# Kernel tuning notes

Hardware: AMD Instinct MI355X
Metric: run time of the kernel (lower is better)

Reference implementation:

```python
import jax, jax.numpy as jnp
import numpy as np

B, T, N, V, C, E = 64, 100, 25, 128, 128, 64
EPS = 1e-5


def setup_inputs() -> dict:
    key = jax.random.key(0)
    ks = jax.random.split(key, 6)
    x = jax.random.normal(ks[0], (B, T, N, V), jnp.float32)
    edge_index = jax.random.randint(ks[1], (2, E), 0, N, dtype=jnp.int64)
    W1 = jax.random.normal(ks[2], (V, C), jnp.float32) * (1.0 / np.sqrt(V))
    b1 = jnp.zeros((C,), jnp.float32)
    W2 = jax.random.normal(ks[3], (C, C), jnp.float32) * (1.0 / np.sqrt(C))
    b2 = jnp.zeros((C,), jnp.float32)
    gamma = jnp.ones((T,), jnp.float32)
    beta = jnp.zeros((T,), jnp.float32)
    return {"x": x, "edge_index": edge_index, "W1": W1, "b1": b1,
            "W2": W2, "b2": b2, "gamma": gamma, "beta": beta}


def _gcn_norm(edge_index, n):
    # GCNConv default: add self-loops, symmetric D^{-1/2} A_hat D^{-1/2} norm.
    loop = jnp.arange(n, dtype=edge_index.dtype)
    src = jnp.concatenate([edge_index[0], loop])  # [E + N]
    tgt = jnp.concatenate([edge_index[1], loop])
    deg = jnp.zeros((n,), jnp.float32).at[tgt].add(1.0)
    dis = jax.lax.rsqrt(deg)  # deg >= 1 due to self-loops
    return src, tgt, dis[src] * dis[tgt]


def _gcn_layer(h, W, b, src, tgt, norm):
    # h: [G, N, Cin] -> [G, N, Cout]; linear then gather-scale-scatter aggregate.
    h = jnp.einsum('gnc,cd->gnd', h, W)
    msg = h[:, src, :] * norm[None, :, None]          # [G, E+N, Cout]
    out = jnp.zeros_like(h).at[:, tgt, :].add(msg)    # scatter-add to targets
    return out + b


def reference(x, edge_index, W1, b1, W2, b2, gamma, beta):
    Bv, Tv, Nv, Vv = x.shape
    h = x.reshape(Bv * Tv, Nv, Vv)  # B*T independent graphs, shared edge_index
    src, tgt, norm = _gcn_norm(edge_index, Nv)
    h = _gcn_layer(h, W1, b1, src, tgt, norm)
    h = _gcn_layer(h, W2, b2, src, tgt, norm)
    y = h.reshape(Bv, Tv, Nv, -1)
    # BatchNorm2d(T) in training mode: batch stats over (B, N, C) per T-channel.
    mean = y.mean(axis=(0, 2, 3), keepdims=True)
    var = y.var(axis=(0, 2, 3), keepdims=True)  # biased, matches torch normalization
    y = (y - mean) * jax.lax.rsqrt(var + EPS)
    y = y * gamma[None, :, None, None] + beta[None, :, None, None]
    return jax.nn.relu(y)
```

## Files before the change

kernel.cpp:

```cpp
#include <hip/hip_runtime.h>

#define T_DIM   100
#define N_NODES 25
#define C_DIM   128
#define G_TOTAL 6400
#define GNV     3200
#define TOT_ELEM 20480000
#define CNT_PER_T 204800.0f

#define WS_A2P  0
#define WS_RS1  640
#define WS_BW   768
#define WS_SUM  1024
#define WS_SSQ  1152
#define WS_W12T 2048
#define WS_HB   16384

#define YSTR  36
#define YGSTR (128 * YSTR)

typedef __attribute__((ext_vector_type(8))) short short8;
typedef __attribute__((ext_vector_type(4))) float f32x4;

__device__ __forceinline__ unsigned short f2bf(float f) {
  unsigned int u = __float_as_uint(f);
  u += 0x7FFFu + ((u >> 16) & 1u);
  return (unsigned short)(u >> 16);
}
__device__ __forceinline__ float bf2f(unsigned short h) {
  return __uint_as_float(((unsigned int)h) << 16);
}
__device__ __forceinline__ unsigned int pack2bf(float a, float b) {
  return (unsigned int)f2bf(a) | ((unsigned int)f2bf(b) << 16);
}

__global__ void k_pre(const int* __restrict__ edge, const float* __restrict__ W1,
                      const float* __restrict__ W2, const float* __restrict__ b1,
                      float* __restrict__ wsf) {
  __shared__ float sA[N_NODES * N_NODES];
  __shared__ float sA2[N_NODES * N_NODES];
  __shared__ float sdeg[N_NODES];
  __shared__ float sdis[N_NODES];
  const int tid = threadIdx.x;

  if (blockIdx.x < 64) {
    int j = blockIdx.x * 256 + tid;
    int c = j & 127, v = j >> 7;
    float acc = 0.f;
#pragma unroll 8
    for (int u = 0; u < 128; u++) acc = fmaf(W1[v * 128 + u], W2[u * 128 + c], acc);
    ((unsigned short*)(wsf + WS_W12T))[c * 128 + v] = f2bf(acc);
    if (j < 128) {
      float a2 = 0.f;
      for (int u = 0; u < 128; u++) a2 = fmaf(W2[u * 128 + j], b1[u], a2);
      wsf[WS_BW + j] = a2;
    }
    return;
  }

  if (tid < N_NODES) sdeg[tid] = 0.f;
  for (int j = tid; j < N_NODES * N_NODES; j += 256) sA[j] = 0.f;
  __syncthreads();
  if (tid < 64) atomicAdd(&sdeg[edge[64 + tid]], 1.f);
  __syncthreads();
  if (tid < N_NODES) sdis[tid] = rsqrtf(sdeg[tid] + 1.f);
  __syncthreads();
  if (tid < 64) {
    int s = edge[tid], tg = edge[64 + tid];
    atomicAdd(&sA[tg * N_NODES + s], sdis[s] * sdis[tg]);
  }
  __syncthreads();
  if (tid < N_NODES) atomicAdd(&sA[tid * N_NODES + tid], sdis[tid] * sdis[tid]);
  __syncthreads();
  for (int j = tid; j < N_NODES * N_NODES; j += 256) {
    int n = j / N_NODES, m = j - n * N_NODES;
    float acc = 0.f;
    for (int k = 0; k < N_NODES; k++) acc = fmaf(sA[n * N_NODES + k], sA[k * N_NODES + m], acc);
    sA2[j] = acc;
  }
  __syncthreads();
  for (int j = tid; j < 1024; j += 256) {
    int m = j >> 5, k = j & 31;
    float v = (m < N_NODES && k < N_NODES) ? sA2[m * N_NODES + k] : 0.f;
    ((unsigned short*)(wsf + WS_A2P))[j] = f2bf(v);
  }
  if (tid < N_NODES) {
    float rs = 0.f;
    for (int m = 0; m < N_NODES; m++) rs += sA[tid * N_NODES + m];
    wsf[WS_RS1 + tid] = rs;
  }
  if (tid < T_DIM) { wsf[WS_SUM + tid] = 0.f; wsf[WS_SSQ + tid] = 0.f; }
}

template <int BF16H>
__device__ __forceinline__ void k_main_body(const float* __restrict__ x,
                                            const float* __restrict__ b2,
                                            const float* __restrict__ wsc,
                                            float* __restrict__ stats,
                                            unsigned short* __restrict__ hb,
                                            float* __restrict__ outf) {
  __shared__ __align__(16) unsigned short LB[4 * YGSTR];
  __shared__ float sBW[128];
  __shared__ float sB2[128];
  __shared__ float rs1[32];
  __shared__ float red[8];
  const int tid = threadIdx.x;
  const int bid = blockIdx.x;
  const int t = bid % T_DIM;
  const int bq = bid / T_DIM;
  const int wv = tid >> 6, lane = tid & 63, quad = lane >> 4, l16 = lane & 15;

  if (tid < 128) {
    sBW[tid] = wsc[WS_BW + tid];
    if (tid < N_NODES) rs1[tid] = wsc[WS_RS1 + tid];
  } else {
    sB2[tid - 128] = b2[tid - 128];
  }
  for (int j = tid; j < 12 * 128; j += 256) {
    int pr = j >> 7;
    int g = pr / 3, rr = pr - (pr / 3) * 3;
    LB[(g * 28 + 25 + rr) * 128 + (j & 127)] = 0;
  }

  {
    const float* xb = x + (bq * 4 * T_DIM + t) * GNV;
    for (int idx = tid; idx < 1600; idx += 256) {
      int row = idx >> 4;
      int c8  = (idx & 15) << 3;
      int g = (row * 41) >> 10;
      int n = row - g * 25;
      const float4* xp = (const float4*)(xb + g * (T_DIM * GNV) + n * 128 + c8);
      float4 f0 = xp[0], f1 = xp[1];
      uint4 w;
      w.x = pack2bf(f0.x, f0.y); w.y = pack2bf(f0.z, f0.w);
      w.z = pack2bf(f1.x, f1.y); w.w = pack2bf(f1.z, f1.w);
      int r = g * 28 + n;
      *(uint4*)&LB[r * 128 + (c8 ^ ((r & 15) << 3))] = w;
    }
  }

  short8 bfr[2][4];
  {
    const unsigned short* Wg = (const unsigned short*)(wsc + WS_W12T);
#pragma unroll
    for (int nt = 0; nt < 2; nt++) {
      const short8* rp = (const short8*)&Wg[(wv * 32 + nt * 16 + l16) * 128];
#pragma unroll
      for (int ks = 0; ks < 4; ks++) bfr[nt][ks] = rp[(ks << 2) | quad];
    }
  }
  __syncthreads();

  f32x4 acc[7][2];
#pragma unroll
  for (int mt = 0; mt < 7; mt++)
#pragma unroll
    for (int nt = 0; nt < 2; nt++)
#pragma unroll
      for (int r = 0; r < 4; r++) acc[mt][nt][r] = 0.f;

#pragma unroll
  for (int ks = 0; ks < 4; ks++) {
    const int cc = (ks << 2) | quad;
#pragma unroll
    for (int mt = 0; mt < 7; mt++) {
      int arow = mt * 16 + l16;
      short8 afr = *(const short8*)&LB[arow * 128 + ((cc ^ (arow & 15)) << 3)];
#pragma unroll
      for (int nt = 0; nt < 2; nt++)
        acc[mt][nt] = __builtin_amdgcn_mfma_f32_16x16x32_bf16(afr, bfr[nt][ks], acc[mt][nt], 0, 0, 0);
    }
  }
  __syncthreads();

#pragma unroll
  for (int mt = 0; mt < 7; mt++) {
    int row0 = mt * 16 + quad * 4;
    int g = row0 / 28;
    int rl = row0 - g * 28;
#pragma unroll
    for (int nt = 0; nt < 2; nt++) {
      int c = wv * 32 + nt * 16 + l16;
      uint2 p;
      p.x = pack2bf(acc[mt][nt][0], acc[mt][nt][1]);
      p.y = pack2bf(acc[mt][nt][2], acc[mt][nt][3]);
      *(uint2*)&LB[g * YGSTR + c * YSTR + rl] = p;
    }
  }
  {
    uint2 z; z.x = 0u; z.y = 0u;
    for (int j = tid; j < 512; j += 256) {
      int g = j >> 7, c = j & 127;
      *(uint2*)&LB[g * YGSTR + c * YSTR + 28] = z;
    }
  }
  __syncthreads();

  const unsigned short* A2p = (const unsigned short*)(wsc + WS_A2P);
  short8 a2f[2];
#pragma unroll
  for (int mt2 = 0; mt2 < 2; mt2++)
    a2f[mt2] = *(const short8*)&A2p[(mt2 * 16 + l16) * 32 + quad * 8];

  const int obase = ((bq * 4 + wv) * T_DIM + t) * GNV;
  float sum = 0.f, ssq = 0.f;
#pragma unroll
  for (int half = 0; half < 2; half++) {
    f32x4 acc2[2][4];
#pragma unroll
    for (int mt2 = 0; mt2 < 2; mt2++)
#pragma unroll
      for (int nt = 0; nt < 4; nt++)
#pragma unroll
        for (int r = 0; r < 4; r++) acc2[mt2][nt][r] = 0.f;

#pragma unroll
    for (int nt = 0; nt < 4; nt++) {
      int c = (half * 4 + nt) * 16 + l16;
      int base = wv * YGSTR + c * YSTR + quad * 8;
      uint2 lo = *(const uint2*)&LB[base];
      uint2 hi = *(const uint2*)&LB[base + 4];
      uint4 w; w.x = lo.x; w.y = lo.y; w.z = hi.x; w.w = hi.y;
      short8 bf = __builtin_bit_cast(short8, w);
#pragma unroll
      for (int mt2 = 0; mt2 < 2; mt2++)
        acc2[mt2][nt] = __builtin_amdgcn_mfma_f32_16x16x32_bf16(a2f[mt2], bf, acc2[mt2][nt], 0, 0, 0);
    }
#pragma unroll
    for (int mt2 = 0; mt2 < 2; mt2++) {
#pragma unroll
      for (int nt = 0; nt < 4; nt++) {
        int c = (half * 4 + nt) * 16 + l16;
        float bw = sBW[c], bb = sB2[c];
#pragma unroll
        for (int r = 0; r < 4; r++) {
          int m = mt2 * 16 + quad * 4 + r;
          if (m < N_NODES) {
            float v = acc2[mt2][nt][r] + rs1[m] * bw + bb;
            if (BF16H) {
              unsigned short hv = f2bf(v);
              float vq = bf2f(hv);
              hb[obase + m * 128 + c] = hv;
              sum += vq;
              ssq += vq * vq;
            } else {
              outf[obase + m * 128 + c] = v;
              sum += v;
              ssq += v * v;
            }
          }
        }
      }
    }
  }

#pragma unroll
  for (int off = 32; off > 0; off >>= 1) {
    sum += __shfl_down(sum, off, 64);
    ssq += __shfl_down(ssq, off, 64);
  }
  if (lane == 0) { red[wv] = sum; red[4 + wv] = ssq; }
  __syncthreads();
  if (tid == 0) {
    atomicAdd(&stats[t], red[0] + red[1] + red[2] + red[3]);
    atomicAdd(&stats[128 + t], red[4] + red[5] + red[6] + red[7]);
  }
}

__global__ __launch_bounds__(256, 4) void k_main_h(const float* __restrict__ x,
                                                   const float* __restrict__ b2,
                                                   const float* __restrict__ wsc,
                                                   float* __restrict__ stats,
                                                   unsigned short* __restrict__ hb) {
  k_main_body<1>(x, b2, wsc, stats, hb, nullptr);
}

__global__ __launch_bounds__(256, 4) void k_main_f(const float* __restrict__ x,
                                                   const float* __restrict__ b2,
                                                   const float* __restrict__ wsc,
                                                   float* __restrict__ stats,
                                                   float* __restrict__ outf) {
  k_main_body<0>(x, b2, wsc, stats, nullptr, outf);
}

__global__ __launch_bounds__(256) void k_norm_h(const unsigned short* __restrict__ hb,
                                                const float* __restrict__ stats,
                                                const float* __restrict__ gamma,
                                                const float* __restrict__ beta,
                                                float* __restrict__ out) {
  const int i8 = (blockIdx.x * 256 + threadIdx.x) * 8;
  const int t = (i8 / GNV) % T_DIM;
  const float inv = 1.f / CNT_PER_T;
  float s = stats[t], q = stats[128 + t];
  float mean = s * inv;
  float var = fmaf(q, inv, -mean * mean);
  float rstd = rsqrtf(var + 1e-5f);
  float gm = gamma[t] * rstd;
  float bt = fmaf(-mean, gm, beta[t]);
  uint4 hw = *(const uint4*)(hb + i8);
  float4 o0, o1;
  o0.x = fmaxf(fmaf(bf2f((unsigned short)(hw.x & 0xFFFF)), gm, bt), 0.f);
  o0.y = fmaxf(fmaf(bf2f((unsigned short)(hw.x >> 16)),    gm, bt), 0.f);
  o0.z = fmaxf(fmaf(bf2f((unsigned short)(hw.y & 0xFFFF)), gm, bt), 0.f);
  o0.w = fmaxf(fmaf(bf2f((unsigned short)(hw.y >> 16)),    gm, bt), 0.f);
  o1.x = fmaxf(fmaf(bf2f((unsigned short)(hw.z & 0xFFFF)), gm, bt), 0.f);
  o1.y = fmaxf(fmaf(bf2f((unsigned short)(hw.z >> 16)),    gm, bt), 0.f);
  o1.z = fmaxf(fmaf(bf2f((unsigned short)(hw.w & 0xFFFF)), gm, bt), 0.f);
  o1.w = fmaxf(fmaf(bf2f((unsigned short)(hw.w >> 16)),    gm, bt), 0.f);
  *(float4*)(out + i8) = o0;
  *(float4*)(out + i8 + 4) = o1;
}

#define NORM_STR  1280000
__global__ __launch_bounds__(256) void k_norm_f(float* __restrict__ out,
                                                const float* __restrict__ stats,
                                                const float* __restrict__ gamma,
                                                const float* __restrict__ beta) {
  const int i0 = blockIdx.x * 256 + threadIdx.x;
  const float inv = 1.f / CNT_PER_T;
  float4 h[4];
  float g[4], bb[4];
  int base[4];
#pragma unroll
  for (int k = 0; k < 4; k++) {
    int i4 = i0 + k * NORM_STR;
    base[k] = i4 * 4;
    int t = (base[k] / GNV) % T_DIM;
    float s = stats[t], q = stats[128 + t];
    float mean = s * inv;
    float var = fmaf(q, inv, -mean * mean);
    float rstd = rsqrtf(var + 1e-5f);
    g[k] = gamma[t] * rstd;
    bb[k] = fmaf(-mean, g[k], beta[t]);
    h[k] = *(const float4*)(out + base[k]);
  }
#pragma unroll
  for (int k = 0; k < 4; k++) {
    float4 v = h[k];
    v.x = fmaxf(fmaf(v.x, g[k], bb[k]), 0.f);
    v.y = fmaxf(fmaf(v.y, g[k], bb[k]), 0.f);
    v.z = fmaxf(fmaf(v.z, g[k], bb[k]), 0.f);
    v.w = fmaxf(fmaf(v.w, g[k], bb[k]), 0.f);
    *(float4*)(out + base[k]) = v;
  }
}

extern "C" void kernel_launch(void* const* d_in, const int* in_sizes, int n_in,
                              void* d_out, int out_size, void* d_ws, size_t ws_size,
                              hipStream_t stream) {
  const float* x     = (const float*)d_in[0];
  const int*   edge  = (const int*)d_in[1];
  const float* W1    = (const float*)d_in[2];
  const float* b1    = (const float*)d_in[3];
  const float* W2    = (const float*)d_in[4];
  const float* b2    = (const float*)d_in[5];
  const float* gamma = (const float*)d_in[6];
  const float* beta  = (const float*)d_in[7];
  float* out = (float*)d_out;
  float* wsf = (float*)d_ws;

  k_pre<<<65, 256, 0, stream>>>(edge, W1, W2, b1, wsf);

  const size_t need = (size_t)WS_HB * 4 + (size_t)TOT_ELEM * 2;
  if (ws_size >= need) {
    unsigned short* hb = (unsigned short*)(wsf + WS_HB);
    k_main_h<<<G_TOTAL / 4, 256, 0, stream>>>(x, b2, wsf, wsf + WS_SUM, hb);
    k_norm_h<<<TOT_ELEM / (256 * 8), 256, 0, stream>>>(hb, wsf + WS_SUM, gamma, beta, out);
  } else {
    k_main_f<<<G_TOTAL / 4, 256, 0, stream>>>(x, b2, wsf, wsf + WS_SUM, out);
    k_norm_f<<<NORM_STR / 256, 256, 0, stream>>>(out, wsf + WS_SUM, gamma, beta);
  }
}
```

Before: 199.3 us.

## Process two graph groups per block, prefetching second group's x during first stage-2

The bf16 main kernel now handles two groups of four graphs per block, with half as many blocks. The second group's x is loaded into registers while the first group's second GCN stage and epilogue run, hiding global load latency behind MFMA work. x loads and output stores now use nontemporal hints, and the normalization kernel handles 16 elements per thread instead of 8. In exchange the kernel holds more registers for the prefetch buffer and launches fewer blocks, which can lower occupancy and leave the grid less balanced.

```diff
diff --git a/kernel.cpp b/kernel.cpp
--- a/kernel.cpp
+++ b/kernel.cpp
@@ -92,13 +92,283 @@
   if (tid < T_DIM) { wsf[WS_SUM + tid] = 0.f; wsf[WS_SSQ + tid] = 0.f; }
 }
 
-template <int BF16H>
-__device__ __forceinline__ void k_main_body(const float* __restrict__ x,
-                                            const float* __restrict__ b2,
-                                            const float* __restrict__ wsc,
-                                            float* __restrict__ stats,
-                                            unsigned short* __restrict__ hb,
-                                            float* __restrict__ outf) {
+__device__ __forceinline__ void load_bfr(const unsigned short* __restrict__ Wg,
+                                         int wv, int quad, int l16, short8 bfr[2][4]) {
+#pragma unroll
+  for (int nt = 0; nt < 2; nt++) {
+    const short8* rp = (const short8*)&Wg[(wv * 32 + nt * 16 + l16) * 128];
+#pragma unroll
+    for (int ks = 0; ks < 4; ks++) bfr[nt][ks] = rp[(ks << 2) | quad];
+  }
+}
+
+__device__ __forceinline__ void load_a2f(const unsigned short* __restrict__ A2p,
+                                         int quad, int l16, short8 a2f[2]) {
+#pragma unroll
+  for (int mt2 = 0; mt2 < 2; mt2++)
+    a2f[mt2] = *(const short8*)&A2p[(mt2 * 16 + l16) * 32 + quad * 8];
+}
+
+__device__ __forceinline__ void stage_x_global(unsigned short* __restrict__ LB,
+                                               const float* __restrict__ xb, int tid) {
+  for (int j = tid; j < 12 * 128; j += 256) {
+    int pr = j >> 7;
+    int g = pr / 3, rr = pr - (pr / 3) * 3;
+    LB[(g * 28 + 25 + rr) * 128 + (j & 127)] = 0;
+  }
+  for (int idx = tid; idx < 1600; idx += 256) {
+    int row = idx >> 4;
+    int c8  = (idx & 15) << 3;
+    int g = (row * 41) >> 10;
+    int n = row - g * 25;
+    const f32x4* xp = (const f32x4*)(xb + g * (T_DIM * GNV) + n * 128 + c8);
+    f32x4 f0 = __builtin_nontemporal_load(xp);
+    f32x4 f1 = __builtin_nontemporal_load(xp + 1);
+    uint4 w;
+    w.x = pack2bf(f0[0], f0[1]); w.y = pack2bf(f0[2], f0[3]);
+    w.z = pack2bf(f1[0], f1[1]); w.w = pack2bf(f1[2], f1[3]);
+    int r = g * 28 + n;
+    *(uint4*)&LB[r * 128 + (c8 ^ ((r & 15) << 3))] = w;
+  }
+}
+
+__device__ __forceinline__ void do_stage1(const unsigned short* __restrict__ LB,
+                                          const short8 bfr[2][4], int quad, int l16,
+                                          f32x4 acc[7][2]) {
+#pragma unroll
+  for (int mt = 0; mt < 7; mt++)
+#pragma unroll
+    for (int nt = 0; nt < 2; nt++)
+#pragma unroll
+      for (int r = 0; r < 4; r++) acc[mt][nt][r] = 0.f;
+#pragma unroll
+  for (int ks = 0; ks < 4; ks++) {
+    const int cc = (ks << 2) | quad;
+#pragma unroll
+    for (int mt = 0; mt < 7; mt++) {
+      int arow = mt * 16 + l16;
+      short8 afr = *(const short8*)&LB[arow * 128 + ((cc ^ (arow & 15)) << 3)];
+#pragma unroll
+      for (int nt = 0; nt < 2; nt++)
+        acc[mt][nt] = __builtin_amdgcn_mfma_f32_16x16x32_bf16(afr, bfr[nt][ks], acc[mt][nt], 0, 0, 0);
+    }
+  }
+}
+
+__device__ __forceinline__ void write_yt(unsigned short* __restrict__ LB,
+                                         const f32x4 acc[7][2], int wv, int quad,
+                                         int l16, int tid) {
+#pragma unroll
+  for (int mt = 0; mt < 7; mt++) {
+    int row0 = mt * 16 + quad * 4;
+    int g = row0 / 28;
+    int rl = row0 - g * 28;
+#pragma unroll
+    for (int nt = 0; nt < 2; nt++) {
+      int c = wv * 32 + nt * 16 + l16;
+      uint2 p;
+      p.x = pack2bf(acc[mt][nt][0], acc[mt][nt][1]);
+      p.y = pack2bf(acc[mt][nt][2], acc[mt][nt][3]);
+      *(uint2*)&LB[g * YGSTR + c * YSTR + rl] = p;
+    }
+  }
+  uint2 z; z.x = 0u; z.y = 0u;
+  for (int j = tid; j < 512; j += 256) {
+    int g = j >> 7, c = j & 127;
+    *(uint2*)&LB[g * YGSTR + c * YSTR + 28] = z;
+  }
+}
+
+__device__ __forceinline__ void do_stage2_epi(const unsigned short* __restrict__ LB,
+    const short8 a2f[2], const float* __restrict__ sBW, const float* __restrict__ sB2,
+    const float* __restrict__ rs1, unsigned short* __restrict__ hb, int obase,
+    int wv, int quad, int l16, float& sum, float& ssq) {
+#pragma unroll
+  for (int half = 0; half < 2; half++) {
+    f32x4 acc2[2][4];
+#pragma unroll
+    for (int mt2 = 0; mt2 < 2; mt2++)
+#pragma unroll
+      for (int nt = 0; nt < 4; nt++)
+#pragma unroll
+        for (int r = 0; r < 4; r++) acc2[mt2][nt][r] = 0.f;
+
+#pragma unroll
+    for (int nt = 0; nt < 4; nt++) {
+      int c = (half * 4 + nt) * 16 + l16;
+      int base = wv * YGSTR + c * YSTR + quad * 8;
+      uint2 lo = *(const uint2*)&LB[base];
+      uint2 hi = *(const uint2*)&LB[base + 4];
+      uint4 w; w.x = lo.x; w.y = lo.y; w.z = hi.x; w.w = hi.y;
+      short8 bf = __builtin_bit_cast(short8, w);
+#pragma unroll
+      for (int mt2 = 0; mt2 < 2; mt2++)
+        acc2[mt2][nt] = __builtin_amdgcn_mfma_f32_16x16x32_bf16(a2f[mt2], bf, acc2[mt2][nt], 0, 0, 0);
+    }
+#pragma unroll
+    for (int mt2 = 0; mt2 < 2; mt2++) {
+#pragma unroll
+      for (int nt = 0; nt < 4; nt++) {
+        int c = (half * 4 + nt) * 16 + l16;
+        float bw = sBW[c], bb = sB2[c];
+#pragma unroll
+        for (int r = 0; r < 4; r++) {
+          int m = mt2 * 16 + quad * 4 + r;
+          if (m < N_NODES) {
+            float v = acc2[mt2][nt][r] + rs1[m] * bw + bb;
+            unsigned short hv = f2bf(v);
+            float vq = bf2f(hv);
+            hb[obase + m * 128 + c] = hv;
+            sum += vq;
+            ssq += vq * vq;
+          }
+        }
+      }
+    }
+  }
+}
+
+__global__ __launch_bounds__(256, 4) void k_main_h2(const float* __restrict__ x,
+                                                    const float* __restrict__ b2,
+                                                    const float* __restrict__ wsc,
+                                                    float* __restrict__ stats,
+                                                    unsigned short* __restrict__ hb) {
+  __shared__ __align__(16) unsigned short LB[4 * YGSTR];
+  __shared__ float sBW[128];
+  __shared__ float sB2[128];
+  __shared__ float rs1[32];
+  __shared__ float red[8];
+  const int tid = threadIdx.x;
+  const int bid = blockIdx.x;
+  const int t = bid % T_DIM;
+  const int bqA = bid / T_DIM;
+  const int bqB = bqA + 8;
+  const int wv = tid >> 6, lane = tid & 63, quad = lane >> 4, l16 = lane & 15;
+  const unsigned short* Wg = (const unsigned short*)(wsc + WS_W12T);
+  const unsigned short* A2p = (const unsigned short*)(wsc + WS_A2P);
+
+  if (tid < 128) {
+    sBW[tid] = wsc[WS_BW + tid];
+    if (tid < N_NODES) rs1[tid] = wsc[WS_RS1 + tid];
+  } else {
+    sB2[tid - 128] = b2[tid - 128];
+  }
+
+  stage_x_global(LB, x + (bqA * 4 * T_DIM + t) * GNV, tid);
+  short8 bfr[2][4];
+  load_bfr(Wg, wv, quad, l16, bfr);
+  __syncthreads();
+
+  f32x4 acc[7][2];
+  do_stage1(LB, bfr, quad, l16, acc);
+  __syncthreads();
+
+  write_yt(LB, acc, wv, quad, l16, tid);
+  __syncthreads();
+
+  uint4 stB[7];
+  const int cnB = (tid < 64) ? 7 : 6;
+  {
+    const float* xbB = x + (bqB * 4 * T_DIM + t) * GNV;
+#pragma unroll
+    for (int i = 0; i < 7; i++) {
+      if (i < cnB) {
+        int idx = tid + (i << 8);
+        int row = idx >> 4, c8 = (idx & 15) << 3;
+        int g = (row * 41) >> 10, n = row - g * 25;
+        const f32x4* xp = (const f32x4*)(xbB + g * (T_DIM * GNV) + n * 128 + c8);
+        f32x4 f0 = __builtin_nontemporal_load(xp);
+        f32x4 f1 = __builtin_nontemporal_load(xp + 1);
+        uint4 w;
+        w.x = pack2bf(f0[0], f0[1]); w.y = pack2bf(f0[2], f0[3]);
+        w.z = pack2bf(f1[0], f1[1]); w.w = pack2bf(f1[2], f1[3]);
+        stB[i] = w;
+      }
+    }
+  }
+
+  short8 a2f[2];
+  load_a2f(A2p, quad, l16, a2f);
+  float sum = 0.f, ssq = 0.f;
+  do_stage2_epi(LB, a2f, sBW, sB2, rs1, hb,
+                ((bqA * 4 + wv) * T_DIM + t) * GNV, wv, quad, l16, sum, ssq);
+  __syncthreads();
+
+  for (int j = tid; j < 12 * 128; j += 256) {
+    int pr = j >> 7;
+    int g = pr / 3, rr = pr - (pr / 3) * 3;
+    LB[(g * 28 + 25 + rr) * 128 + (j & 127)] = 0;
+  }
+#pragma unroll
+  for (int i = 0; i < 7; i++) {
+    if (i < cnB) {
+      int idx = tid + (i << 8);
+      int row = idx >> 4, c8 = (idx & 15) << 3;
+      int g = (row * 41) >> 10, n = row - g * 25;
+      int r = g * 28 + n;
+      *(uint4*)&LB[r * 128 + (c8 ^ ((r & 15) << 3))] = stB[i];
+    }
+  }
+  load_bfr(Wg, wv, quad, l16, bfr);
+  __syncthreads();
+
+  do_stage1(LB, bfr, quad, l16, acc);
+  __syncthreads();
+
+  write_yt(LB, acc, wv, quad, l16, tid);
+  __syncthreads();
+
+  load_a2f(A2p, quad, l16, a2f);
+  do_stage2_epi(LB, a2f, sBW, sB2, rs1, hb,
+                ((bqB * 4 + wv) * T_DIM + t) * GNV, wv, quad, l16, sum, ssq);
+
+#pragma unroll
+  for (int off = 32; off > 0; off >>= 1) {
+    sum += __shfl_down(sum, off, 64);
+    ssq += __shfl_down(ssq, off, 64);
+  }
+  if (lane == 0) { red[wv] = sum; red[4 + wv] = ssq; }
+  __syncthreads();
+  if (tid == 0) {
+    atomicAdd(&stats[t], red[0] + red[1] + red[2] + red[3]);
+    atomicAdd(&stats[128 + t], red[4] + red[5] + red[6] + red[7]);
+  }
+}
+
+__global__ __launch_bounds__(256) void k_norm_h(const unsigned short* __restrict__ hb,
+                                                const float* __restrict__ stats,
+                                                const float* __restrict__ gamma,
+                                                const float* __restrict__ beta,
+                                                float* __restrict__ out) {
+  const int i16 = (blockIdx.x * 256 + threadIdx.x) * 16;
+  const int t = (i16 / GNV) % T_DIM;
+  const float inv = 1.f / CNT_PER_T;
+  float s = stats[t], q = stats[128 + t];
+  float mean = s * inv;
+  float var = fmaf(q, inv, -mean * mean);
+  float rstd = rsqrtf(var + 1e-5f);
+  float gm = gamma[t] * rstd;
+  float bt = fmaf(-mean, gm, beta[t]);
+  uint4 h0 = *(const uint4*)(hb + i16);
+  uint4 h1 = *(const uint4*)(hb + i16 + 8);
+  unsigned int hw[8] = {h0.x, h0.y, h0.z, h0.w, h1.x, h1.y, h1.z, h1.w};
+#pragma unroll
+  for (int k = 0; k < 4; k++) {
+    unsigned int a = hw[2 * k], b = hw[2 * k + 1];
+    f32x4 o;
+    o[0] = fmaxf(fmaf(bf2f((unsigned short)(a & 0xFFFF)), gm, bt), 0.f);
+    o[1] = fmaxf(fmaf(bf2f((unsigned short)(a >> 16)),    gm, bt), 0.f);
+    o[2] = fmaxf(fmaf(bf2f((unsigned short)(b & 0xFFFF)), gm, bt), 0.f);
+    o[3] = fmaxf(fmaf(bf2f((unsigned short)(b >> 16)),    gm, bt), 0.f);
+    __builtin_nontemporal_store(o, (f32x4*)(out + i16 + 4 * k));
+  }
+}
+
+__global__ __launch_bounds__(256, 4) void k_main_f(const float* __restrict__ x,
+                                                   const float* __restrict__ b2,
+                                                   const float* __restrict__ wsc,
+                                                   float* __restrict__ stats,
+                                                   float* __restrict__ outf) {
   __shared__ __align__(16) unsigned short LB[4 * YGSTR];
   __shared__ float sBW[128];
   __shared__ float sB2[128];
@@ -109,6 +379,8 @@
   const int t = bid % T_DIM;
   const int bq = bid / T_DIM;
   const int wv = tid >> 6, lane = tid & 63, quad = lane >> 4, l16 = lane & 15;
+  const unsigned short* Wg = (const unsigned short*)(wsc + WS_W12T);
+  const unsigned short* A2p = (const unsigned short*)(wsc + WS_A2P);
 
   if (tid < 128) {
     sBW[tid] = wsc[WS_BW + tid];
@@ -116,92 +388,17 @@
   } else {
     sB2[tid - 128] = b2[tid - 128];
   }
-  for (int j = tid; j < 12 * 128; j += 256) {
-    int pr = j >> 7;
-    int g = pr / 3, rr = pr - (pr / 3) * 3;
-    LB[(g * 28 + 25 + rr) * 128 + (j & 127)] = 0;
-  }
-
-  {
-    const float* xb = x + (bq * 4 * T_DIM + t) * GNV;
-    for (int idx = tid; idx < 1600; idx += 256) {
-      int row = idx >> 4;
-      int c8  = (idx & 15) << 3;
-      int g = (row * 41) >> 10;
-      int n = row - g * 25;
-      const float4* xp = (const float4*)(xb + g * (T_DIM * GNV) + n * 128 + c8);
-      float4 f0 = xp[0], f1 = xp[1];
-      uint4 w;
-      w.x = pack2bf(f0.x, f0.y); w.y = pack2bf(f0.z, f0.w);
-      w.z = pack2bf(f1.x, f1.y); w.w = pack2bf(f1.z, f1.w);
-      int r = g * 28 + n;
-      *(uint4*)&LB[r * 128 + (c8 ^ ((r & 15) << 3))] = w;
-    }
-  }
-
+  stage_x_global(LB, x + (bq * 4 * T_DIM + t) * GNV, tid);
   short8 bfr[2][4];
-  {
-    const unsigned short* Wg = (const unsigned short*)(wsc + WS_W12T);
-#pragma unroll
-    for (int nt = 0; nt < 2; nt++) {
-      const short8* rp = (const short8*)&Wg[(wv * 32 + nt * 16 + l16) * 128];
-#pragma unroll
-      for (int ks = 0; ks < 4; ks++) bfr[nt][ks] = rp[(ks << 2) | quad];
-    }
-  }
-  __syncthreads();
-
+  load_bfr(Wg, wv, quad, l16, bfr);
+  __syncthreads();
   f32x4 acc[7][2];
-#pragma unroll
-  for (int mt = 0; mt < 7; mt++)
-#pragma unroll
-    for (int nt = 0; nt < 2; nt++)
-#pragma unroll
-      for (int r = 0; r < 4; r++) acc[mt][nt][r] = 0.f;
-
-#pragma unroll
-  for (int ks = 0; ks < 4; ks++) {
-    const int cc = (ks << 2) | quad;
-#pragma unroll
-    for (int mt = 0; mt < 7; mt++) {
-      int arow = mt * 16 + l16;
-      short8 afr = *(const short8*)&LB[arow * 128 + ((cc ^ (arow & 15)) << 3)];
-#pragma unroll
-      for (int nt = 0; nt < 2; nt++)
-        acc[mt][nt] = __builtin_amdgcn_mfma_f32_16x16x32_bf16(afr, bfr[nt][ks], acc[mt][nt], 0, 0, 0);
-    }
-  }
-  __syncthreads();
-
-#pragma unroll
-  for (int mt = 0; mt < 7; mt++) {
-    int row0 = mt * 16 + quad * 4;
-    int g = row0 / 28;
-    int rl = row0 - g * 28;
-#pragma unroll
-    for (int nt = 0; nt < 2; nt++) {
-      int c = wv * 32 + nt * 16 + l16;
-      uint2 p;
-      p.x = pack2bf(acc[mt][nt][0], acc[mt][nt][1]);
-      p.y = pack2bf(acc[mt][nt][2], acc[mt][nt][3]);
-      *(uint2*)&LB[g * YGSTR + c * YSTR + rl] = p;
-    }
-  }
-  {
-    uint2 z; z.x = 0u; z.y = 0u;
-    for (int j = tid; j < 512; j += 256) {
-      int g = j >> 7, c = j & 127;
-      *(uint2*)&LB[g * YGSTR + c * YSTR + 28] = z;
-    }
-  }
-  __syncthreads();
-
-  const unsigned short* A2p = (const unsigned short*)(wsc + WS_A2P);
+  do_stage1(LB, bfr, quad, l16, acc);
+  __syncthreads();
+  write_yt(LB, acc, wv, quad, l16, tid);
+  __syncthreads();
   short8 a2f[2];
-#pragma unroll
-  for (int mt2 = 0; mt2 < 2; mt2++)
-    a2f[mt2] = *(const short8*)&A2p[(mt2 * 16 + l16) * 32 + quad * 8];
-
+  load_a2f(A2p, quad, l16, a2f);
   const int obase = ((bq * 4 + wv) * T_DIM + t) * GNV;
   float sum = 0.f, ssq = 0.f;
 #pragma unroll
@@ -213,7 +410,6 @@
       for (int nt = 0; nt < 4; nt++)
 #pragma unroll
         for (int r = 0; r < 4; r++) acc2[mt2][nt][r] = 0.f;
-
 #pragma unroll
     for (int nt = 0; nt < 4; nt++) {
       int c = (half * 4 + nt) * 16 + l16;
@@ -237,23 +433,14 @@
           int m = mt2 * 16 + quad * 4 + r;
           if (m < N_NODES) {
             float v = acc2[mt2][nt][r] + rs1[m] * bw + bb;
-            if (BF16H) {
-              unsigned short hv = f2bf(v);
-              float vq = bf2f(hv);
-              hb[obase + m * 128 + c] = hv;
-              sum += vq;
-              ssq += vq * vq;
-            } else {
-              outf[obase + m * 128 + c] = v;
-              sum += v;
-              ssq += v * v;
-            }
+            outf[obase + m * 128 + c] = v;
+            sum += v;
+            ssq += v * v;
           }
         }
       }
     }
   }
-
 #pragma unroll
   for (int off = 32; off > 0; off >>= 1) {
     sum += __shfl_down(sum, off, 64);
@@ -265,50 +452,6 @@
     atomicAdd(&stats[t], red[0] + red[1] + red[2] + red[3]);
     atomicAdd(&stats[128 + t], red[4] + red[5] + red[6] + red[7]);
   }
-}
-
-__global__ __launch_bounds__(256, 4) void k_main_h(const float* __restrict__ x,
-                                                   const float* __restrict__ b2,
-                                                   const float* __restrict__ wsc,
-                                                   float* __restrict__ stats,
-                                                   unsigned short* __restrict__ hb) {
-  k_main_body<1>(x, b2, wsc, stats, hb, nullptr);
-}
-
-__global__ __launch_bounds__(256, 4) void k_main_f(const float* __restrict__ x,
-                                                   const float* __restrict__ b2,
-                                                   const float* __restrict__ wsc,
-                                                   float* __restrict__ stats,
-                                                   float* __restrict__ outf) {
-  k_main_body<0>(x, b2, wsc, stats, nullptr, outf);
-}
-
-__global__ __launch_bounds__(256) void k_norm_h(const unsigned short* __restrict__ hb,
-                                                const float* __restrict__ stats,
-                                                const float* __restrict__ gamma,
-                                                const float* __restrict__ beta,
-                                                float* __restrict__ out) {
-  const int i8 = (blockIdx.x * 256 + threadIdx.x) * 8;
-  const int t = (i8 / GNV) % T_DIM;
-  const float inv = 1.f / CNT_PER_T;
-  float s = stats[t], q = stats[128 + t];
-  float mean = s * inv;
-  float var = fmaf(q, inv, -mean * mean);
-  float rstd = rsqrtf(var + 1e-5f);
-  float gm = gamma[t] * rstd;
-  float bt = fmaf(-mean, gm, beta[t]);
-  uint4 hw = *(const uint4*)(hb + i8);
-  float4 o0, o1;
-  o0.x = fmaxf(fmaf(bf2f((unsigned short)(hw.x & 0xFFFF)), gm, bt), 0.f);
-  o0.y = fmaxf(fmaf(bf2f((unsigned short)(hw.x >> 16)),    gm, bt), 0.f);
-  o0.z = fmaxf(fmaf(bf2f((unsigned short)(hw.y & 0xFFFF)), gm, bt), 0.f);
-  o0.w = fmaxf(fmaf(bf2f((unsigned short)(hw.y >> 16)),    gm, bt), 0.f);
-  o1.x = fmaxf(fmaf(bf2f((unsigned short)(hw.z & 0xFFFF)), gm, bt), 0.f);
-  o1.y = fmaxf(fmaf(bf2f((unsigned short)(hw.z >> 16)),    gm, bt), 0.f);
-  o1.z = fmaxf(fmaf(bf2f((unsigned short)(hw.w & 0xFFFF)), gm, bt), 0.f);
-  o1.w = fmaxf(fmaf(bf2f((unsigned short)(hw.w >> 16)),    gm, bt), 0.f);
-  *(float4*)(out + i8) = o0;
-  *(float4*)(out + i8 + 4) = o1;
 }
 
 #define NORM_STR  1280000
@@ -364,8 +507,8 @@
   const size_t need = (size_t)WS_HB * 4 + (size_t)TOT_ELEM * 2;
   if (ws_size >= need) {
     unsigned short* hb = (unsigned short*)(wsf + WS_HB);
-    k_main_h<<<G_TOTAL / 4, 256, 0, stream>>>(x, b2, wsf, wsf + WS_SUM, hb);
-    k_norm_h<<<TOT_ELEM / (256 * 8), 256, 0, stream>>>(hb, wsf + WS_SUM, gamma, beta, out);
+    k_main_h2<<<G_TOTAL / 8, 256, 0, stream>>>(x, b2, wsf, wsf + WS_SUM, hb);
+    k_norm_h<<<TOT_ELEM / (256 * 16), 256, 0, stream>>>(hb, wsf + WS_SUM, gamma, beta, out);
   } else {
     k_main_f<<<G_TOTAL / 4, 256, 0, stream>>>(x, b2, wsf, wsf + WS_SUM, out);
     k_norm_f<<<NORM_STR / 256, 256, 0, stream>>>(out, wsf + WS_SUM, gamma, beta);
```

Result: slower. 258.4 us (+29.7%).
